# Performance work log

Hardware: AMD Instinct MI355X
Metric: run time of the kernel (lower is better)

The kernel has to match this reference:

```python
import jax, jax.numpy as jnp
import numpy as np
import math

NUM_HEADS = 16
HEAD_DIM = 32  # latent_dim // num_heads = 512 // 16


def rope(x, pos):
    # x: (B, H, S, Dh); half-split rotary embedding, theta=10000
    d = x.shape[-1] // 2
    inv_freq = 1.0 / (10000.0 ** (jnp.arange(d, dtype=jnp.float32) / d))
    ang = pos.astype(jnp.float32)[:, None] * inv_freq[None, :]  # (S, d)
    cos, sin = jnp.cos(ang), jnp.sin(ang)
    x1, x2 = x[..., :d], x[..., d:]
    return jnp.concatenate([x1 * cos - x2 * sin, x1 * sin + x2 * cos], axis=-1)


def setup_inputs() -> dict:
    key = jax.random.key(0)
    ks = jax.random.split(key, 16)
    B, L, KV_PREV = 1, 2048, 2048
    D, D_KV = 2048, 512
    s = lambda fan_in: 1.0 / math.sqrt(fan_in)
    return {
        "x": jax.random.normal(ks[0], (B, L, D), jnp.float32),
        "z_cache": jax.random.normal(ks[1], (B, KV_PREV, D_KV), jnp.float32),
        "valid_lens": jax.random.randint(ks[2], (B, L), 1, KV_PREV + L, jnp.int32),
        "W_latent": jax.random.normal(ks[3], (D, D_KV), jnp.float32) * s(D),
        "b_latent": jnp.zeros((D_KV,), jnp.float32),
        "W_q": jax.random.normal(ks[4], (D, NUM_HEADS * HEAD_DIM), jnp.float32) * s(D),
        "b_q": jnp.zeros((NUM_HEADS * HEAD_DIM,), jnp.float32),
        "W_k": jax.random.normal(ks[5], (D_KV, NUM_HEADS * HEAD_DIM), jnp.float32) * s(D_KV),
        "b_k": jnp.zeros((NUM_HEADS * HEAD_DIM,), jnp.float32),
        "W_v": jax.random.normal(ks[6], (D_KV, NUM_HEADS * HEAD_DIM), jnp.float32) * s(D_KV),
        "b_v": jnp.zeros((NUM_HEADS * HEAD_DIM,), jnp.float32),
        "W_o": jax.random.normal(ks[7], (NUM_HEADS * HEAD_DIM, D), jnp.float32) * s(NUM_HEADS * HEAD_DIM),
        "b_o": jnp.zeros((D,), jnp.float32),
    }


def reference(x, z_cache, valid_lens, W_latent, b_latent, W_q, b_q, W_k, b_k, W_v, b_v, W_o, b_o):
    B, L, D = x.shape
    H, Dh = NUM_HEADS, HEAD_DIM
    # latent projection + cache concat
    z_new = x @ W_latent + b_latent                      # (B, L, D_kv)
    z = jnp.concatenate([z_cache, z_new], axis=1)        # (B, KV, D_kv)
    KV = z.shape[1]
    q = (x @ W_q + b_q).reshape(B, L, H, Dh).transpose(0, 2, 1, 3)   # (B,H,L,Dh)
    k = (z @ W_k + b_k).reshape(B, KV, H, Dh).transpose(0, 2, 1, 3)  # (B,H,KV,Dh)
    v = (z @ W_v + b_v).reshape(B, KV, H, Dh).transpose(0, 2, 1, 3)  # (B,H,KV,Dh)
    q = rope(q, jnp.arange(L))
    k = rope(k, jnp.arange(KV))
    scores = jnp.einsum("bhqd,bhkd->bhqk", q, k) / math.sqrt(Dh)     # (B,H,L,KV)
    # faithful: unmasked softmax (returned as attn_weights), then re-masked softmax
    attn_weights = jax.nn.softmax(scores, axis=-1)
    invalid = jnp.arange(KV)[None, None, None, :] >= valid_lens[:, None, :, None]
    masked = jnp.where(invalid, jnp.float32(-10000.0), scores)
    masked_w = jax.nn.softmax(masked, axis=-1)
    heads = jnp.einsum("bhqk,bhkd->bhqd", masked_w, v)               # (B,H,L,Dh)
    heads = heads.transpose(0, 2, 1, 3).reshape(B, L, H * Dh)
    output = heads @ W_o + b_o                                       # (B, L, D)
    return (output, z, attn_weights, scores)
```

## Files before the change

### kernel.cpp

```cpp
#include <hip/hip_runtime.h>
#include <math.h>

#define L_Q     2048
#define KV_PREV 2048
#define KV_TOT  4096
#define DIM     2048
#define D_KV    512
#define NH      16
#define DH      32
#define HDh     512
#define KC      256
#define KQ      (KV_TOT / 4)

typedef short bf16x8 __attribute__((ext_vector_type(8)));
typedef short bf16x4 __attribute__((ext_vector_type(4)));
typedef float f32x4  __attribute__((ext_vector_type(4)));

__device__ inline short f2bf(float f) {
    unsigned u = __float_as_uint(f);
    u += 0x7fff + ((u >> 16) & 1);
    return (short)(u >> 16);
}

__device__ __constant__ double c_invfreq[16] = {
    1.0, 0.5623413251903491, 0.31622776601683794, 0.17782794100389228,
    0.1, 0.05623413251903491, 0.03162277660168379, 0.017782794100389228,
    0.01, 0.005623413251903491, 0.0031622776601683794, 0.0017782794100389228,
    0.001, 0.0005623413251903491, 0.00031622776601683794, 0.00017782794100389227,
};

__global__ void cvt_bf16(const float* __restrict__ in, short* __restrict__ out, int n8) {
    int i = blockIdx.x * blockDim.x + threadIdx.x;
    if (i >= n8) return;
    float4 a = reinterpret_cast<const float4*>(in)[2 * i];
    float4 b = reinterpret_cast<const float4*>(in)[2 * i + 1];
    union { short s[8]; int4 v; } u;
    u.s[0] = f2bf(a.x); u.s[1] = f2bf(a.y); u.s[2] = f2bf(a.z); u.s[3] = f2bf(a.w);
    u.s[4] = f2bf(b.x); u.s[5] = f2bf(b.y); u.s[6] = f2bf(b.z); u.s[7] = f2bf(b.w);
    reinterpret_cast<int4*>(out)[i] = u.v;
}

__global__ void cvt_copy(const float* __restrict__ src, float* __restrict__ dst,
                         short* __restrict__ dbf, int n8) {
    int i = blockIdx.x * blockDim.x + threadIdx.x;
    if (i >= n8) return;
    float4 a = reinterpret_cast<const float4*>(src)[2 * i];
    float4 b = reinterpret_cast<const float4*>(src)[2 * i + 1];
    reinterpret_cast<float4*>(dst)[2 * i]     = a;
    reinterpret_cast<float4*>(dst)[2 * i + 1] = b;
    union { short s[8]; int4 v; } u;
    u.s[0] = f2bf(a.x); u.s[1] = f2bf(a.y); u.s[2] = f2bf(a.z); u.s[3] = f2bf(a.w);
    u.s[4] = f2bf(b.x); u.s[5] = f2bf(b.y); u.s[6] = f2bf(b.z); u.s[7] = f2bf(b.w);
    reinterpret_cast<int4*>(dbf)[i] = u.v;
}

__global__ __launch_bounds__(256) void tr_cvt(const float* __restrict__ in,
        short* __restrict__ out, int K, int N) {
    __shared__ float tile[32][33];
    int k0 = blockIdx.x * 32, n0 = blockIdx.y * 32;
    int c = threadIdx.x & 31, r0 = threadIdx.x >> 5;
    for (int r = r0; r < 32; r += 8)
        tile[r][c] = in[(size_t)(k0 + r) * N + n0 + c];
    __syncthreads();
    for (int r = r0; r < 32; r += 8)
        out[(size_t)(n0 + r) * K + k0 + c] = f2bf(tile[c][r]);
}

__global__ __launch_bounds__(256) void vt_cvt(const short* __restrict__ v, short* __restrict__ vt) {
    __shared__ short tile[64][34];
    int h = blockIdx.y, kv0 = blockIdx.x * 64;
    int c = threadIdx.x & 31, r0 = threadIdx.x >> 5;
    for (int r = r0; r < 64; r += 8)
        tile[r][c] = v[(size_t)(kv0 + r) * HDh + h * DH + c];
    __syncthreads();
    int l = threadIdx.x & 63, wv = threadIdx.x >> 6;
    for (int d = wv; d < 32; d += 4)
        vt[((size_t)h * DH + d) * KV_TOT + kv0 + l] = tile[l][d];
}

__global__ __launch_bounds__(256) void gemm_bf16(const short* __restrict__ A,
        const short* __restrict__ Bt, const float* __restrict__ bias,
        float* __restrict__ C, short* __restrict__ Cbf, int rope,
        int M, int N, int K)
{
    int t = threadIdx.x, w = t >> 6, l = t & 63, lr = l & 15, lg = l >> 4;
    int m0 = blockIdx.y * 64 + w * 16;
    int n0 = blockIdx.x * 64;
    f32x4 acc[4] = {{0,0,0,0},{0,0,0,0},{0,0,0,0},{0,0,0,0}};
    const short* ap  = A  + (size_t)(m0 + lr) * K + lg * 8;
    const short* bp0 = Bt + (size_t)(n0 + lr) * K + lg * 8;
    #pragma unroll 2
    for (int k0 = 0; k0 < K; k0 += 32) {
        bf16x8 a = *reinterpret_cast<const bf16x8*>(ap + k0);
        #pragma unroll
        for (int j = 0; j < 4; ++j) {
            bf16x8 b = *reinterpret_cast<const bf16x8*>(bp0 + (size_t)j * 16 * K + k0);
            acc[j] = __builtin_amdgcn_mfma_f32_16x16x32_bf16(a, b, acc[j], 0, 0, 0);
        }
    }
    float bs[4];
    #pragma unroll
    for (int j = 0; j < 4; ++j) bs[j] = bias[n0 + j * 16 + lr];

    if (rope) {
        #pragma unroll
        for (int r = 0; r < 4; ++r) {
            int m = m0 + lg * 4 + r;
            float ang = (float)((double)m * c_invfreq[lr]);
            float cs = cosf(ang), sn = sinf(ang);
            size_t rb = (size_t)m * N + n0 + lr;
            float a1 = acc[0][r] + bs[0], a2 = acc[1][r] + bs[1];
            Cbf[rb]      = f2bf(a1 * cs - a2 * sn);
            Cbf[rb + 16] = f2bf(a1 * sn + a2 * cs);
            float b1 = acc[2][r] + bs[2], b2 = acc[3][r] + bs[3];
            Cbf[rb + 32] = f2bf(b1 * cs - b2 * sn);
            Cbf[rb + 48] = f2bf(b1 * sn + b2 * cs);
        }
        return;
    }
    #pragma unroll
    for (int j = 0; j < 4; ++j) {
        int n = n0 + j * 16 + lr;
        #pragma unroll
        for (int r = 0; r < 4; ++r) {
            float v = acc[j][r] + bs[j];
            size_t idx = (size_t)(m0 + lg * 4 + r) * N + n;
            if (C)   C[idx] = v;
            if (Cbf) Cbf[idx] = f2bf(v);
        }
    }
}

__global__ __launch_bounds__(256) void scores_stats(const short* __restrict__ q,
        const short* __restrict__ kmat, const int* __restrict__ vlens,
        float* __restrict__ scores, float* __restrict__ isu_o, float* __restrict__ is2_o)
{
    __shared__ float Sl[4][16][KC + 4];
    __shared__ float red[4][16][2];
    int t = threadIdx.x, w = t >> 6, l = t & 63, lr = l & 15, lg = l >> 4;
    int h = blockIdx.y;
    int qrow = blockIdx.x * 16;
    int myq = qrow + lr;
    bf16x8 bQ = *reinterpret_cast<const bf16x8*>(q + (size_t)myq * HDh + h * DH + lg * 8);
    int vl = vlens[myq];
    const short* kp = kmat + h * DH + lg * 8;
    const float sc = 0.17677669529663687f;
    float su = 0.f, s2 = 0.f;
    const int kb = lg * 4;
    const int kq0 = w * KQ;

    bf16x8 a0 = *reinterpret_cast<const bf16x8*>(kp + (size_t)(kq0 + lr) * HDh);
    bf16x8 a1 = *reinterpret_cast<const bf16x8*>(kp + (size_t)(kq0 + 16 + lr) * HDh);
    for (int c = 0; c < KQ / KC; ++c) {
        int kbase = kq0 + c * KC;
        #pragma unroll
        for (int kt = 0; kt < KC / 32; ++kt) {
            int k0 = kbase + kt * 32;
            int kn = kq0 + ((c * KC + kt * 32 + 32) & (KQ - 1));
            bf16x8 a0n = *reinterpret_cast<const bf16x8*>(kp + (size_t)(kn + lr) * HDh);
            bf16x8 a1n = *reinterpret_cast<const bf16x8*>(kp + (size_t)(kn + 16 + lr) * HDh);
            f32x4 z4 = {0.f, 0.f, 0.f, 0.f};
            f32x4 s0 = __builtin_amdgcn_mfma_f32_16x16x32_bf16(a0, bQ, z4, 0, 0, 0);
            f32x4 s1 = __builtin_amdgcn_mfma_f32_16x16x32_bf16(a1, bQ, z4, 0, 0, 0);
            f32x4 o0, o1;
            #pragma unroll
            for (int r = 0; r < 4; ++r) { o0[r] = s0[r] * sc; o1[r] = s1[r] * sc; }
            *reinterpret_cast<f32x4*>(&Sl[w][lr][kt * 32 + kb])      = o0;
            *reinterpret_cast<f32x4*>(&Sl[w][lr][kt * 32 + 16 + kb]) = o1;
            #pragma unroll
            for (int r = 0; r < 4; ++r) {
                float e0 = __expf(o0[r]), e1 = __expf(o1[r]);
                su += e0 + e1;
                if (k0 + kb + r < vl)      s2 += e0;
                if (k0 + 16 + kb + r < vl) s2 += e1;
            }
            a0 = a0n; a1 = a1n;
        }
        __builtin_amdgcn_s_barrier();
        #pragma unroll
        for (int r = 0; r < 16; ++r) {
            f32x4 v = *reinterpret_cast<const f32x4*>(&Sl[w][r][l * 4]);
            __builtin_nontemporal_store(v, reinterpret_cast<f32x4*>(
                scores + ((size_t)h * L_Q + qrow + r) * KV_TOT + kbase + l * 4));
        }
    }
    su += __shfl_xor(su, 16, 64); su += __shfl_xor(su, 32, 64);
    s2 += __shfl_xor(s2, 16, 64); s2 += __shfl_xor(s2, 32, 64);
    if (lg == 0) { red[w][lr][0] = su; red[w][lr][1] = s2; }
    __syncthreads();
    if (t < 16) {
        float sut = red[0][t][0] + red[1][t][0] + red[2][t][0] + red[3][t][0];
        float s2t = red[0][t][1] + red[1][t][1] + red[2][t][1] + red[3][t][1];
        size_t idx = (size_t)h * L_Q + qrow + t;
        isu_o[idx] = 1.f / sut;
        is2_o[idx] = 1.f / s2t;
    }
}

__global__ __launch_bounds__(256) void attn_pv(const short* __restrict__ q,
        const short* __restrict__ kmat, const int* __restrict__ vlens,
        const float* __restrict__ isu_i, const float* __restrict__ is2_i,
        const short* __restrict__ Vt,
        float* __restrict__ attn, short* __restrict__ heads_bf)
{
    __shared__ float Al[4][16][KC + 4];
    __shared__ short Plds[4][16][72];
    int t = threadIdx.x, w = t >> 6, l = t & 63, lr = l & 15, lg = l >> 4;
    int h = blockIdx.y;
    int qrow = blockIdx.x * 16;
    int myq = qrow + lr;
    bf16x8 bQ = *reinterpret_cast<const bf16x8*>(q + (size_t)myq * HDh + h * DH + lg * 8);
    int vl = vlens[myq];
    size_t sidx = (size_t)h * L_Q + myq;
    float isu = isu_i[sidx], is2 = is2_i[sidx];
    const short* kp  = kmat + h * DH + lg * 8;
    const short* vp0 = Vt + ((size_t)h * DH + lr) * KV_TOT + lg * 8;
    const short* vp1 = vp0 + (size_t)16 * KV_TOT;
    const float sc = 0.17677669529663687f;
    const int kb = lg * 4;
    const int kq0 = w * KQ;
    short* prow = &Plds[w][lr][0];
    f32x4 h0 = {0,0,0,0}, h1 = {0,0,0,0};

    for (int c = 0; c < KQ / KC; ++c) {
        int kbase = kq0 + c * KC;
        #pragma unroll
        for (int g = 0; g < 4; ++g) {
            #pragma unroll
            for (int kt = 0; kt < 4; ++kt) {
                int i = g * 4 + kt;
                bf16x8 aK = *reinterpret_cast<const bf16x8*>(
                    kp + (size_t)(kbase + i * 16 + lr) * HDh);
                f32x4 z4 = {0.f, 0.f, 0.f, 0.f};
                f32x4 s = __builtin_amdgcn_mfma_f32_16x16x32_bf16(aK, bQ, z4, 0, 0, 0);
                f32x4 oa;
                bf16x4 pb;
                #pragma unroll
                for (int r = 0; r < 4; ++r) {
                    float e = __expf(s[r] * sc);
                    oa[r] = e * isu;
                    pb[r] = (kbase + i * 16 + kb + r < vl) ? f2bf(e * is2) : (short)0;
                }
                *reinterpret_cast<f32x4*>(&Al[w][lr][i * 16 + kb]) = oa;
                *reinterpret_cast<bf16x4*>(prow + kt * 16 + kb) = pb;
            }
            #pragma unroll
            for (int kbl = 0; kbl < 2; ++kbl) {
                int kv = kbase + g * 64 + kbl * 32;
                bf16x8 pa = *reinterpret_cast<const bf16x8*>(prow + kbl * 32 + lg * 8);
                bf16x8 b0 = *reinterpret_cast<const bf16x8*>(vp0 + kv);
                bf16x8 b1 = *reinterpret_cast<const bf16x8*>(vp1 + kv);
                h0 = __builtin_amdgcn_mfma_f32_16x16x32_bf16(pa, b0, h0, 0, 0, 0);
                h1 = __builtin_amdgcn_mfma_f32_16x16x32_bf16(pa, b1, h1, 0, 0, 0);
            }
        }
        __builtin_amdgcn_s_barrier();
        #pragma unroll
        for (int r = 0; r < 16; ++r) {
            f32x4 v = *reinterpret_cast<const f32x4*>(&Al[w][r][l * 4]);
            __builtin_nontemporal_store(v, reinterpret_cast<f32x4*>(
                attn + ((size_t)h * L_Q + qrow + r) * KV_TOT + kbase + l * 4));
        }
    }
    __syncthreads();
    float* hst = &Al[0][0][0];
    if (w > 0) {
        *reinterpret_cast<f32x4*>(&hst[((w - 1) * 64 + l) * 8])     = h0;
        *reinterpret_cast<f32x4*>(&hst[((w - 1) * 64 + l) * 8 + 4]) = h1;
    }
    __syncthreads();
    if (w == 0) {
        #pragma unroll
        for (int ww = 0; ww < 3; ++ww) {
            f32x4 g0 = *reinterpret_cast<const f32x4*>(&hst[(ww * 64 + l) * 8]);
            f32x4 g1 = *reinterpret_cast<const f32x4*>(&hst[(ww * 64 + l) * 8 + 4]);
            h0 += g0; h1 += g1;
        }
        #pragma unroll
        for (int r = 0; r < 4; ++r) {
            size_t ho = (size_t)(qrow + lg * 4 + r) * HDh + h * DH + lr;
            heads_bf[ho]      = f2bf(h0[r]);
            heads_bf[ho + 16] = f2bf(h1[r]);
        }
    }
}

extern "C" void kernel_launch(void* const* d_in, const int* in_sizes, int n_in,
                              void* d_out, int out_size, void* d_ws, size_t ws_size,
                              hipStream_t stream) {
    const float* x       = (const float*)d_in[0];
    const float* z_cache = (const float*)d_in[1];
    const int*   vlens   = (const int*)  d_in[2];
    const float* W_lat   = (const float*)d_in[3];
    const float* b_lat   = (const float*)d_in[4];
    const float* W_q     = (const float*)d_in[5];
    const float* b_q     = (const float*)d_in[6];
    const float* W_k     = (const float*)d_in[7];
    const float* b_k     = (const float*)d_in[8];
    const float* W_v     = (const float*)d_in[9];
    const float* b_v     = (const float*)d_in[10];
    const float* W_o     = (const float*)d_in[11];
    const float* b_o     = (const float*)d_in[12];

    float* out        = (float*)d_out;
    float* out_output = out;
    float* out_z      = out_output + (size_t)L_Q * DIM;
    float* out_attn   = out_z + (size_t)KV_TOT * D_KV;
    float* out_scores = out_attn + (size_t)NH * L_Q * KV_TOT;

    float* wf     = (float*)d_ws;
    float* ws_isu = wf;
    float* ws_is2 = ws_isu + (size_t)NH * L_Q;
    short* wsb      = (short*)(ws_is2 + (size_t)NH * L_Q);
    short* x_bf     = wsb;
    short* z_bf     = x_bf + (size_t)L_Q * DIM;
    short* q_bf     = z_bf + (size_t)KV_TOT * D_KV;
    short* k_bf     = q_bf + (size_t)L_Q * HDh;
    short* v_bf     = k_bf + (size_t)KV_TOT * HDh;
    short* Vt       = v_bf + (size_t)KV_TOT * HDh;
    short* heads_bf = Vt + (size_t)NH * DH * KV_TOT;
    short* Wt_lat   = heads_bf + (size_t)L_Q * HDh;
    short* Wt_q     = Wt_lat + (size_t)D_KV * DIM;
    short* Wt_k     = Wt_q + (size_t)HDh * DIM;
    short* Wt_v     = Wt_k + (size_t)HDh * D_KV;
    short* Wt_o     = Wt_v + (size_t)HDh * D_KV;

    cvt_bf16<<<(L_Q * DIM / 8 + 255) / 256, 256, 0, stream>>>(x, x_bf, L_Q * DIM / 8);
    cvt_copy<<<(KV_PREV * D_KV / 8 + 255) / 256, 256, 0, stream>>>(
        z_cache, out_z, z_bf, KV_PREV * D_KV / 8);
    tr_cvt<<<dim3(DIM / 32, D_KV / 32), 256, 0, stream>>>(W_lat, Wt_lat, DIM, D_KV);
    tr_cvt<<<dim3(DIM / 32, HDh / 32), 256, 0, stream>>>(W_q, Wt_q, DIM, HDh);
    tr_cvt<<<dim3(D_KV / 32, HDh / 32), 256, 0, stream>>>(W_k, Wt_k, D_KV, HDh);
    tr_cvt<<<dim3(D_KV / 32, HDh / 32), 256, 0, stream>>>(W_v, Wt_v, D_KV, HDh);
    tr_cvt<<<dim3(HDh / 32, DIM / 32), 256, 0, stream>>>(W_o, Wt_o, HDh, DIM);

    gemm_bf16<<<dim3(D_KV / 64, L_Q / 64), 256, 0, stream>>>(
        x_bf, Wt_lat, b_lat, out_z + (size_t)KV_PREV * D_KV,
        z_bf + (size_t)KV_PREV * D_KV, 0, L_Q, D_KV, DIM);

    gemm_bf16<<<dim3(HDh / 64, L_Q / 64), 256, 0, stream>>>(
        x_bf, Wt_q, b_q, nullptr, q_bf, 1, L_Q, HDh, DIM);
    gemm_bf16<<<dim3(HDh / 64, KV_TOT / 64), 256, 0, stream>>>(
        z_bf, Wt_k, b_k, nullptr, k_bf, 1, KV_TOT, HDh, D_KV);
    gemm_bf16<<<dim3(HDh / 64, KV_TOT / 64), 256, 0, stream>>>(
        z_bf, Wt_v, b_v, nullptr, v_bf, 0, KV_TOT, HDh, D_KV);
    vt_cvt<<<dim3(KV_TOT / 64, NH), 256, 0, stream>>>(v_bf, Vt);

    scores_stats<<<dim3(L_Q / 16, NH), 256, 0, stream>>>(
        q_bf, k_bf, vlens, out_scores, ws_isu, ws_is2);

    attn_pv<<<dim3(L_Q / 16, NH), 256, 0, stream>>>(
        q_bf, k_bf, vlens, ws_isu, ws_is2, Vt, out_attn, heads_bf);

    gemm_bf16<<<dim3(DIM / 64, L_Q / 64), 256, 0, stream>>>(
        heads_bf, Wt_o, b_o, out_output, nullptr, 0, L_Q, DIM, HDh);
}
```

Baseline: 556.7 us.

## Fuse weight transposes, x conversion and paired projection GEMMs into fewer launches

Merges the five weight transpose-convert kernels into one launch, drops the standalone x-to-bf16 conversion by converting fp32 x inside the GEMM load, and pairs the latent/Q and K/V projections into dual GEMM launches that share the A operand. The aim is to cut launch overhead and the extra pass over x, and to put more blocks in flight per launch. In exchange, x is converted once per N-block inside the GEMM, which re-reads the fp32 x, and the K loop is no longer explicitly unrolled.

```diff
diff --git a/kernel.cpp b/kernel.cpp
--- a/kernel.cpp
+++ b/kernel.cpp
@@ -28,17 +28,6 @@
     0.01, 0.005623413251903491, 0.0031622776601683794, 0.0017782794100389228,
     0.001, 0.0005623413251903491, 0.00031622776601683794, 0.00017782794100389227,
 };
-
-__global__ void cvt_bf16(const float* __restrict__ in, short* __restrict__ out, int n8) {
-    int i = blockIdx.x * blockDim.x + threadIdx.x;
-    if (i >= n8) return;
-    float4 a = reinterpret_cast<const float4*>(in)[2 * i];
-    float4 b = reinterpret_cast<const float4*>(in)[2 * i + 1];
-    union { short s[8]; int4 v; } u;
-    u.s[0] = f2bf(a.x); u.s[1] = f2bf(a.y); u.s[2] = f2bf(a.z); u.s[3] = f2bf(a.w);
-    u.s[4] = f2bf(b.x); u.s[5] = f2bf(b.y); u.s[6] = f2bf(b.z); u.s[7] = f2bf(b.w);
-    reinterpret_cast<int4*>(out)[i] = u.v;
-}
 
 __global__ void cvt_copy(const float* __restrict__ src, float* __restrict__ dst,
                          short* __restrict__ dbf, int n8) {
@@ -54,10 +43,22 @@
     reinterpret_cast<int4*>(dbf)[i] = u.v;
 }
 
-__global__ __launch_bounds__(256) void tr_cvt(const float* __restrict__ in,
-        short* __restrict__ out, int K, int N) {
+__global__ __launch_bounds__(256) void tr_cvt_all(
+        const float* __restrict__ W0, const float* __restrict__ W1,
+        const float* __restrict__ W2, const float* __restrict__ W3,
+        const float* __restrict__ W4,
+        short* __restrict__ O0, short* __restrict__ O1, short* __restrict__ O2,
+        short* __restrict__ O3, short* __restrict__ O4) {
     __shared__ float tile[32][33];
-    int k0 = blockIdx.x * 32, n0 = blockIdx.y * 32;
+    int b = blockIdx.x;
+    const float* in; short* out; int K, N;
+    if (b < 1024)      { in = W0; out = O0; K = 2048; N = 512; }
+    else if (b < 2048) { in = W1; out = O1; K = 2048; N = 512;  b -= 1024; }
+    else if (b < 2304) { in = W2; out = O2; K = 512;  N = 512;  b -= 2048; }
+    else if (b < 2560) { in = W3; out = O3; K = 512;  N = 512;  b -= 2304; }
+    else               { in = W4; out = O4; K = 512;  N = 2048; b -= 2560; }
+    int nkb = K / 32;
+    int k0 = (b % nkb) * 32, n0 = (b / nkb) * 32;
     int c = threadIdx.x & 31, r0 = threadIdx.x >> 5;
     for (int r = r0; r < 32; r += 8)
         tile[r][c] = in[(size_t)(k0 + r) * N + n0 + c];
@@ -80,8 +81,7 @@
 
 __global__ __launch_bounds__(256) void gemm_bf16(const short* __restrict__ A,
         const short* __restrict__ Bt, const float* __restrict__ bias,
-        float* __restrict__ C, short* __restrict__ Cbf, int rope,
-        int M, int N, int K)
+        float* __restrict__ C, int M, int N, int K)
 {
     int t = threadIdx.x, w = t >> 6, l = t & 63, lr = l & 15, lg = l >> 4;
     int m0 = blockIdx.y * 64 + w * 16;
@@ -98,6 +98,52 @@
             acc[j] = __builtin_amdgcn_mfma_f32_16x16x32_bf16(a, b, acc[j], 0, 0, 0);
         }
     }
+    #pragma unroll
+    for (int j = 0; j < 4; ++j) {
+        int n = n0 + j * 16 + lr;
+        float bs = bias[n];
+        #pragma unroll
+        for (int r = 0; r < 4; ++r)
+            C[(size_t)(m0 + lg * 4 + r) * N + n] = acc[j][r] + bs;
+    }
+}
+
+__global__ __launch_bounds__(256) void gemm_dual(
+        const float* __restrict__ Af, const short* __restrict__ Ab,
+        const short* __restrict__ Bt0, const float* __restrict__ bias0,
+        float* __restrict__ C0f, short* __restrict__ C0bf, int rope0,
+        const short* __restrict__ Bt1, const float* __restrict__ bias1,
+        float* __restrict__ C1f, short* __restrict__ C1bf, int rope1,
+        int M, int K)
+{
+    int t = threadIdx.x, w = t >> 6, l = t & 63, lr = l & 15, lg = l >> 4;
+    int side = blockIdx.x >> 3;
+    int n0 = (blockIdx.x & 7) * 64;
+    int m0 = blockIdx.y * 64 + w * 16;
+    const short* Bt;  const float* bias;  float* Cf;  short* Cbf;  int rope;
+    if (side == 0) { Bt = Bt0; bias = bias0; Cf = C0f; Cbf = C0bf; rope = rope0; }
+    else           { Bt = Bt1; bias = bias1; Cf = C1f; Cbf = C1bf; rope = rope1; }
+
+    f32x4 acc[4] = {{0,0,0,0},{0,0,0,0},{0,0,0,0},{0,0,0,0}};
+    const float* afp = Af ? Af + (size_t)(m0 + lr) * K + lg * 8 : nullptr;
+    const short* abp = Ab ? Ab + (size_t)(m0 + lr) * K + lg * 8 : nullptr;
+    const short* bp0 = Bt + (size_t)(n0 + lr) * K + lg * 8;
+    for (int k0 = 0; k0 < K; k0 += 32) {
+        bf16x8 a;
+        if (Af) {
+            float4 f0 = *reinterpret_cast<const float4*>(afp + k0);
+            float4 f1 = *reinterpret_cast<const float4*>(afp + k0 + 4);
+            a[0] = f2bf(f0.x); a[1] = f2bf(f0.y); a[2] = f2bf(f0.z); a[3] = f2bf(f0.w);
+            a[4] = f2bf(f1.x); a[5] = f2bf(f1.y); a[6] = f2bf(f1.z); a[7] = f2bf(f1.w);
+        } else {
+            a = *reinterpret_cast<const bf16x8*>(abp + k0);
+        }
+        #pragma unroll
+        for (int j = 0; j < 4; ++j) {
+            bf16x8 b = *reinterpret_cast<const bf16x8*>(bp0 + (size_t)j * 16 * K + k0);
+            acc[j] = __builtin_amdgcn_mfma_f32_16x16x32_bf16(a, b, acc[j], 0, 0, 0);
+        }
+    }
     float bs[4];
     #pragma unroll
     for (int j = 0; j < 4; ++j) bs[j] = bias[n0 + j * 16 + lr];
@@ -108,7 +154,7 @@
             int m = m0 + lg * 4 + r;
             float ang = (float)((double)m * c_invfreq[lr]);
             float cs = cosf(ang), sn = sinf(ang);
-            size_t rb = (size_t)m * N + n0 + lr;
+            size_t rb = (size_t)m * 512 + n0 + lr;
             float a1 = acc[0][r] + bs[0], a2 = acc[1][r] + bs[1];
             Cbf[rb]      = f2bf(a1 * cs - a2 * sn);
             Cbf[rb + 16] = f2bf(a1 * sn + a2 * cs);
@@ -124,8 +170,8 @@
         #pragma unroll
         for (int r = 0; r < 4; ++r) {
             float v = acc[j][r] + bs[j];
-            size_t idx = (size_t)(m0 + lg * 4 + r) * N + n;
-            if (C)   C[idx] = v;
+            size_t idx = (size_t)(m0 + lg * 4 + r) * 512 + n;
+            if (Cf)  Cf[idx]  = v;
             if (Cbf) Cbf[idx] = f2bf(v);
         }
     }
@@ -312,8 +358,7 @@
     float* ws_isu = wf;
     float* ws_is2 = ws_isu + (size_t)NH * L_Q;
     short* wsb      = (short*)(ws_is2 + (size_t)NH * L_Q);
-    short* x_bf     = wsb;
-    short* z_bf     = x_bf + (size_t)L_Q * DIM;
+    short* z_bf     = wsb;
     short* q_bf     = z_bf + (size_t)KV_TOT * D_KV;
     short* k_bf     = q_bf + (size_t)L_Q * HDh;
     short* v_bf     = k_bf + (size_t)KV_TOT * HDh;
@@ -325,25 +370,22 @@
     short* Wt_v     = Wt_k + (size_t)HDh * D_KV;
     short* Wt_o     = Wt_v + (size_t)HDh * D_KV;
 
-    cvt_bf16<<<(L_Q * DIM / 8 + 255) / 256, 256, 0, stream>>>(x, x_bf, L_Q * DIM / 8);
     cvt_copy<<<(KV_PREV * D_KV / 8 + 255) / 256, 256, 0, stream>>>(
         z_cache, out_z, z_bf, KV_PREV * D_KV / 8);
-    tr_cvt<<<dim3(DIM / 32, D_KV / 32), 256, 0, stream>>>(W_lat, Wt_lat, DIM, D_KV);
-    tr_cvt<<<dim3(DIM / 32, HDh / 32), 256, 0, stream>>>(W_q, Wt_q, DIM, HDh);
-    tr_cvt<<<dim3(D_KV / 32, HDh / 32), 256, 0, stream>>>(W_k, Wt_k, D_KV, HDh);
-    tr_cvt<<<dim3(D_KV / 32, HDh / 32), 256, 0, stream>>>(W_v, Wt_v, D_KV, HDh);
-    tr_cvt<<<dim3(HDh / 32, DIM / 32), 256, 0, stream>>>(W_o, Wt_o, HDh, DIM);
-
-    gemm_bf16<<<dim3(D_KV / 64, L_Q / 64), 256, 0, stream>>>(
-        x_bf, Wt_lat, b_lat, out_z + (size_t)KV_PREV * D_KV,
-        z_bf + (size_t)KV_PREV * D_KV, 0, L_Q, D_KV, DIM);
-
-    gemm_bf16<<<dim3(HDh / 64, L_Q / 64), 256, 0, stream>>>(
-        x_bf, Wt_q, b_q, nullptr, q_bf, 1, L_Q, HDh, DIM);
-    gemm_bf16<<<dim3(HDh / 64, KV_TOT / 64), 256, 0, stream>>>(
-        z_bf, Wt_k, b_k, nullptr, k_bf, 1, KV_TOT, HDh, D_KV);
-    gemm_bf16<<<dim3(HDh / 64, KV_TOT / 64), 256, 0, stream>>>(
-        z_bf, Wt_v, b_v, nullptr, v_bf, 0, KV_TOT, HDh, D_KV);
+    tr_cvt_all<<<3584, 256, 0, stream>>>(W_lat, W_q, W_k, W_v, W_o,
+                                         Wt_lat, Wt_q, Wt_k, Wt_v, Wt_o);
+
+    gemm_dual<<<dim3(16, L_Q / 64), 256, 0, stream>>>(
+        x, nullptr,
+        Wt_lat, b_lat, out_z + (size_t)KV_PREV * D_KV, z_bf + (size_t)KV_PREV * D_KV, 0,
+        Wt_q, b_q, nullptr, q_bf, 1,
+        L_Q, DIM);
+
+    gemm_dual<<<dim3(16, KV_TOT / 64), 256, 0, stream>>>(
+        nullptr, z_bf,
+        Wt_k, b_k, nullptr, k_bf, 1,
+        Wt_v, b_v, nullptr, v_bf, 0,
+        KV_TOT, D_KV);
     vt_cvt<<<dim3(KV_TOT / 64, NH), 256, 0, stream>>>(v_bf, Vt);
 
     scores_stats<<<dim3(L_Q / 16, NH), 256, 0, stream>>>(
@@ -353,5 +395,5 @@
         q_bf, k_bf, vlens, ws_isu, ws_is2, Vt, out_attn, heads_bf);
 
     gemm_bf16<<<dim3(DIM / 64, L_Q / 64), 256, 0, stream>>>(
-        heads_bf, Wt_o, b_o, out_output, nullptr, 0, L_Q, DIM, HDh);
-}
+        heads_bf, Wt_o, b_o, out_output, L_Q, DIM, HDh);
+}
```

Measured after the change: 523.7 us. 5.9% less time.
